# Optimization experiments

Hardware: AMD Instinct MI355X
Metric: run time of the kernel (lower is better)

The kernel has to match this reference:

```python
import jax, jax.numpy as jnp
import numpy as np

UPDATE_SCALE = 1.0
DIST_THRESHOLD = 3.0
W_INJECT = 1.0
W_PIXEL = 1.0
EPS = 1e-8
BIG = 1e6  # sentinel coordinate for masked-out gt points


def extract_zc(sdf):
    """Zero crossings along vertical then horizontal neighbor pairs.
    Returns pts [Ncand,2] float, mask [Ncand] bool (fixed-size, masked)."""
    H, W = sdf.shape
    ii = jnp.arange(H, dtype=sdf.dtype)
    jj = jnp.arange(W, dtype=sdf.dtype)
    # vertical pairs (i,j)-(i+1,j): shape [H-1, W]
    v1, v2 = sdf[:-1, :], sdf[1:, :]
    a = jnp.abs(v1) / (jnp.abs(v1) + jnp.abs(v2) + EPS)
    i0 = ii[:-1, None]
    rv = jnp.where(v1 == 0, i0, jnp.where(v2 == 0, i0 + 1.0, i0 + a))
    cv = jnp.broadcast_to(jj[None, :], v1.shape)
    mv = (v1 == 0) | (v2 == 0) | (v1 * v2 < 0)
    # horizontal pairs (i,j)-(i,j+1): shape [H, W-1]
    h1, h2 = sdf[:, :-1], sdf[:, 1:]
    b = jnp.abs(h1) / (jnp.abs(h1) + jnp.abs(h2) + EPS)
    j0 = jj[None, :-1]
    ch = jnp.where(h1 == 0, j0, jnp.where(h2 == 0, j0 + 1.0, j0 + b))
    rh = jnp.broadcast_to(ii[:, None], h1.shape)
    mh = (h1 == 0) | (h2 == 0) | (h1 * h2 < 0)
    pts = jnp.concatenate([
        jnp.stack([rv.ravel(), cv.ravel()], axis=1),
        jnp.stack([rh.ravel(), ch.ravel()], axis=1)], axis=0)
    mask = jnp.concatenate([mv.ravel(), mh.ravel()], axis=0)
    return pts, mask


def compute_normals(sdf):
    # central differences, one-sided at edges -> [H,W,2]
    gr = jnp.concatenate([sdf[1:2] - sdf[0:1], (sdf[2:] - sdf[:-2]) / 2.0,
                          sdf[-1:] - sdf[-2:-1]], axis=0)
    gc = jnp.concatenate([sdf[:, 1:2] - sdf[:, 0:1], (sdf[:, 2:] - sdf[:, :-2]) / 2.0,
                          sdf[:, -1:] - sdf[:, -2:-1]], axis=1)
    return jnp.stack([gr, gc], axis=2)


def _corners(pts, H, W):
    r, c = pts[:, 0], pts[:, 1]
    r0 = jnp.clip(jnp.floor(r).astype(jnp.int32), 0, H - 1)
    c0 = jnp.clip(jnp.floor(c).astype(jnp.int32), 0, W - 1)
    r1 = jnp.clip(r0 + 1, 0, H - 1)
    c1 = jnp.clip(c0 + 1, 0, W - 1)
    ar = r - r0.astype(r.dtype)
    ac = c - c0.astype(c.dtype)
    wa = (1 - ar) * (1 - ac); wb = (1 - ar) * ac
    wc = ar * (1 - ac); wd = ar * ac
    return r0, c0, r1, c1, wa, wb, wc, wd


def bilinear_gather(img, pts):
    H, W = img.shape[0], img.shape[1]
    r0, c0, r1, c1, wa, wb, wc, wd = _corners(pts, H, W)
    if img.ndim == 3:
        wa, wb, wc, wd = wa[:, None], wb[:, None], wc[:, None], wd[:, None]
    return (img[r0, c0] * wa + img[r0, c1] * wb
            + img[r1, c0] * wc + img[r1, c1] * wd)


def one_image(pred, gt):
    H, W = pred.shape
    gt_pts, gt_m = extract_zc(jax.lax.stop_gradient(gt))
    pr_pts, pr_m = extract_zc(jax.lax.stop_gradient(pred))
    # bilinearly sampled, normalized normals at pred zero crossings
    normals = compute_normals(pred)                         # [H,W,2]
    n = bilinear_gather(normals, pr_pts)                    # [M,2]
    n = n / (jnp.linalg.norm(n, axis=1, keepdims=True) + 1e-8)
    # brute-force NN of each pred ZC point in gt ZC points (masked gt -> far away)
    gp = jnp.where(gt_m[:, None], gt_pts, BIG)              # [N,2]
    d2 = ((pr_pts ** 2).sum(1)[:, None] + (gp ** 2).sum(1)[None, :]
          - 2.0 * pr_pts @ gp.T)                            # [M,N]
    d2 = jnp.maximum(d2, 0.0)
    idx = jnp.argmin(d2, axis=1)
    md2 = jnp.min(d2, axis=1)
    near = gp[idx]                                          # [M,2]
    contrib = pr_m & (md2 <= DIST_THRESHOLD ** 2)
    dirv = near - pr_pts
    dot = jnp.where(contrib, (dirv * n).sum(1) * UPDATE_SCALE, 0.0)
    # bilinear scatter of dot into dSDF (weights vanish exactly where torch skips out-of-range)
    r0, c0, r1, c1, wa, wb, wc, wd = _corners(pr_pts, H, W)
    dSDF = jnp.zeros_like(pred)
    dSDF = (dSDF.at[r0, c0].add(dot * wa)
                 .at[r0, c1].add(dot * wb)
                 .at[r1, c0].add(dot * wc)
                 .at[r1, c1].add(dot * wd))
    dSDF = jax.lax.stop_gradient(dSDF)
    inj = jnp.sum(pred * dSDF)
    vals = bilinear_gather(pred, pr_pts)                    # [M]
    pix = jnp.sum(jnp.where(pr_m, vals, 0.0))
    return inj, pix


def setup_inputs() -> dict:
    key = jax.random.key(0)
    k1, k2 = jax.random.split(key)
    B, H, W = 1, 96, 96
    pred_sdf = jax.random.normal(k1, (B, H, W), dtype=jnp.float32)
    gt_sdf = jax.random.normal(k2, (B, H, W), dtype=jnp.float32)
    return {"pred_sdf": pred_sdf, "gt_sdf": gt_sdf}


def reference(pred_sdf, gt_sdf):
    inj, pix = jax.vmap(one_image)(pred_sdf, gt_sdf)
    inject = inj.mean()
    pixel = pix.mean()
    return W_INJECT * inject + W_PIXEL * pixel
```

## Files before the change

kernel.cpp:

```cpp
#include <hip/hip_runtime.h>
#include <math.h>

#pragma clang fp contract(off)

#define HH 96
#define WW 96
#define NV 9120
#define NC 18240
#define NPIX 9216
#define NCELL 9216
#define SLOTS 6
#define NBLK 4560
#define BIGF 1000000.0f

__global__ void k_prep(const float* __restrict__ PR, const float* __restrict__ GT,
                       float* __restrict__ N,
                       float* prR, float* prC, int* prM,
                       float* gtR, float* gtC,
                       int* counts, float4* cells){
#pragma clang fp contract(off)
  int t = blockIdx.x*256 + threadIdx.x;
  if (t < NPIX){
    int i = t / WW, j = t % WW;
    float gr, gc;
    if (i == 0)         gr = PR[WW+j] - PR[j];
    else if (i == HH-1) gr = PR[(HH-1)*WW+j] - PR[(HH-2)*WW+j];
    else                gr = (PR[(i+1)*WW+j] - PR[(i-1)*WW+j]) / 2.0f;
    if (j == 0)         gc = PR[i*WW+1] - PR[i*WW];
    else if (j == WW-1) gc = PR[i*WW+WW-1] - PR[i*WW+WW-2];
    else                gc = (PR[i*WW+j+1] - PR[i*WW+j-1]) / 2.0f;
    N[t*2] = gr; N[t*2+1] = gc;
  }
  if (t >= 2*NC) return;
  const float* S = (t < NC) ? PR : GT;
  int u = (t < NC) ? t : t - NC;
  float v1, v2, r, c;
  if (u < NV){
    int i0 = u / WW, j = u % WW;
    v1 = S[i0*WW+j]; v2 = S[(i0+1)*WW+j];
    float a1 = fabsf(v1), a2 = fabsf(v2);
    float den = (a1 + a2) + 1e-8f;
    float a = a1 / den;
    float i0f = (float)i0;
    r = (v1 == 0.0f) ? i0f : ((v2 == 0.0f) ? (i0f + 1.0f) : (i0f + a));
    c = (float)j;
  } else {
    int u2 = u - NV;
    int i = u2 / (WW-1), j0 = u2 % (WW-1);
    v1 = S[i*WW+j0]; v2 = S[i*WW+j0+1];
    float a1 = fabsf(v1), a2 = fabsf(v2);
    float den = (a1 + a2) + 1e-8f;
    float b = a1 / den;
    float j0f = (float)j0;
    c = (v1 == 0.0f) ? j0f : ((v2 == 0.0f) ? (j0f + 1.0f) : (j0f + b));
    r = (float)i;
  }
  int m = (v1 == 0.0f) || (v2 == 0.0f) || ((v1*v2) < 0.0f);
  if (t < NC){ prR[u] = r; prC[u] = c; prM[u] = m; }
  else {
    float gr = m ? r : BIGF;
    float gc = m ? c : BIGF;
    gtR[u] = gr; gtC[u] = gc;
    if (m){
      int fr = (int)floorf(r); if (fr < 0) fr = 0; if (fr > HH-1) fr = HH-1;
      int fc = (int)floorf(c); if (fc < 0) fc = 0; if (fc > WW-1) fc = WW-1;
      int cell = fr*WW + fc;
      int slot = atomicAdd(&counts[cell], 1);
      if (slot < SLOTS){
        float sg = (r*r) + (c*c);
        cells[cell*SLOTS + slot] = make_float4(r, c, sg, __int_as_float(u));
      }
    }
  }
}

__global__ __launch_bounds__(256) void k_nndot(
    const float* __restrict__ PR, const float* __restrict__ N,
    const float* __restrict__ prR, const float* __restrict__ prC,
    const int* __restrict__ prM,
    const float* __restrict__ gtR, const float* __restrict__ gtC,
    const int* __restrict__ counts, const float4* __restrict__ cells,
    float* dotA, double* pvPart){
#pragma clang fp contract(off)
  int lane = threadIdx.x & 63, wid = threadIdx.x >> 6;
  int k = blockIdx.x*4 + wid;
  float rp = prR[k], cp = prC[k];
  float sp = (rp*rp) + (cp*cp);
  int fr = (int)floorf(rp), fc = (int)floorf(cp);
  float best = 3.4e38f; int bjg = 0x7fffffff;
  for (int idx = lane; idx < 81; idx += 64){
    int ci = fr + idx/9 - 4;
    int cj = fc + idx%9 - 4;
    if (ci >= 0 && ci < HH && cj >= 0 && cj < WW){
      int cell = ci*WW + cj;
      int n = counts[cell]; if (n > SLOTS) n = SLOTS;
      for (int s = 0; s < n; ++s){
        float4 g = cells[cell*SLOTS + s];
        float cross = fmaf(cp, g.y, rp*g.x);
        float d2 = (sp + g.z) - (2.0f*cross);
        d2 = fmaxf(d2, 0.0f);
        int jg = __float_as_int(g.w);
        if ((d2 < best) || ((d2 == best) && (jg < bjg))){ best = d2; bjg = jg; }
      }
    }
  }
  for (int off = 32; off; off >>= 1){
    float ob = __shfl_xor(best, off, 64);
    int   oj = __shfl_xor(bjg,  off, 64);
    if ((ob < best) || ((ob == best) && (oj < bjg))){ best = ob; bjg = oj; }
  }
  __shared__ double sb[4];
  if (lane == 0){
    if (bjg < 0 || bjg > NC-1) bjg = 0;
    int r0 = (int)floorf(rp); if (r0 < 0) r0 = 0; if (r0 > HH-1) r0 = HH-1;
    int c0 = (int)floorf(cp); if (c0 < 0) c0 = 0; if (c0 > WW-1) c0 = WW-1;
    int r1 = r0 + 1; if (r1 > HH-1) r1 = HH-1;
    int c1 = c0 + 1; if (c1 > WW-1) c1 = WW-1;
    float ar = rp - (float)r0, ac = cp - (float)c0;
    float omr = 1.0f - ar, omc = 1.0f - ac;
    float wa = omr*omc, wb = omr*ac, wc = ar*omc, wd = ar*ac;
    float nr = (((N[(r0*WW+c0)*2]*wa) + (N[(r0*WW+c1)*2]*wb))
               + (N[(r1*WW+c0)*2]*wc)) + (N[(r1*WW+c1)*2]*wd);
    float nc = (((N[(r0*WW+c0)*2+1]*wa) + (N[(r0*WW+c1)*2+1]*wb))
               + (N[(r1*WW+c0)*2+1]*wc)) + (N[(r1*WW+c1)*2+1]*wd);
    float nrm = sqrtf((nr*nr) + (nc*nc));
    float den = nrm + 1e-8f;
    float nru = nr / den, ncu = nc / den;
    float dr = gtR[bjg] - rp;
    float dc = gtC[bjg] - cp;
    float dotv = (dr*nru) + (dc*ncu);
    int m = prM[k];
    int contrib = m && (best <= 9.0f);
    dotA[k] = contrib ? dotv : 0.0f;
    float vals = (((PR[r0*WW+c0]*wa) + (PR[r0*WW+c1]*wb))
                 + (PR[r1*WW+c0]*wc)) + (PR[r1*WW+c1]*wd);
    sb[wid] = m ? (double)vals : 0.0;
  }
  __syncthreads();
  if (threadIdx.x == 0) pvPart[blockIdx.x] = (sb[0]+sb[1])+(sb[2]+sb[3]);
}

__global__ __launch_bounds__(64) void k_pixel(const float* __restrict__ PR,
                        const float* __restrict__ prR, const float* __restrict__ prC,
                        const float* __restrict__ dotA, float* tmp){
#pragma clang fp contract(off)
  int p = blockIdx.x*64 + threadIdx.x;
  if (p >= NPIX) return;
  int i = p / WW, j = p % WW;
  float s = 0.0f;
  for (int i0 = i-1; i0 <= i; ++i0){
    if (i0 < 0 || i0 > HH-2) continue;
    int k = i0*WW + j;
    float r = prR[k];
    int r0 = (int)floorf(r);
    if (r0 == i){
      float ar = r - (float)r0;
      float w = 1.0f - ar;
      s = s + (dotA[k] * w);
    }
  }
  for (int j0 = j-1; j0 <= j; ++j0){
    if (j0 < 0 || j0 > WW-2) continue;
    int k = NV + i*(WW-1) + j0;
    float c = prC[k];
    int c0 = (int)floorf(c);
    if (c0 == j){
      float ac = c - (float)c0;
      float w = 1.0f - ac;
      s = s + (dotA[k] * w);
    }
  }
  for (int j0 = j-2; j0 <= j-1; ++j0){
    if (j0 < 0 || j0 > WW-2) continue;
    int k = NV + i*(WW-1) + j0;
    float c = prC[k];
    int c0 = (int)floorf(c);
    if (c0 == j-1){
      float ac = c - (float)c0;
      s = s + (dotA[k] * ac);
    }
  }
  for (int i0 = i-2; i0 <= i-1; ++i0){
    if (i0 < 0 || i0 > HH-2) continue;
    int k = i0*WW + j;
    float r = prR[k];
    int r0 = (int)floorf(r);
    if (r0 == i-1){
      float ar = r - (float)r0;
      s = s + (dotA[k] * ar);
    }
  }
  tmp[p] = PR[p] * s;
}

__global__ void k_final(const float* __restrict__ tmp,
                        const double* __restrict__ pvPart, float* out){
#pragma clang fp contract(off)
  __shared__ float buf[128];
  __shared__ double dbuf[128];
  int t = threadIdx.x;
  const float4* a4 = (const float4*)(tmp + t*72);
  float4 x = a4[0], y = a4[1];
  float r0=x.x, r1=x.y, r2=x.z, r3=x.w, r4=y.x, r5=y.y, r6=y.z, r7=y.w;
  for (int i4 = 2; i4 < 18; i4 += 2){
    float4 u = a4[i4], v = a4[i4+1];
    r0 += u.x; r1 += u.y; r2 += u.z; r3 += u.w;
    r4 += v.x; r5 += v.y; r6 += v.z; r7 += v.w;
  }
  buf[t] = ((r0+r1)+(r2+r3)) + ((r4+r5)+(r6+r7));
  double pv = 0.0;
  for (int i = t; i < NBLK; i += 128) pv += pvPart[i];
  dbuf[t] = pv;
  __syncthreads();
  for (int st = 1; st < 128; st <<= 1){
    if ((t & (2*st - 1)) == 0){
      buf[t]  = buf[t]  + buf[t+st];
      dbuf[t] = dbuf[t] + dbuf[t+st];
    }
    __syncthreads();
  }
  if (t == 0){
    float inj = buf[0];
    float pix = (float)dbuf[0];
    out[0] = inj + pix;
  }
}

extern "C" void kernel_launch(void* const* d_in, const int* in_sizes, int n_in,
                              void* d_out, int out_size, void* d_ws, size_t ws_size,
                              hipStream_t stream){
  const float* pred = (const float*)d_in[0];
  const float* gt   = (const float*)d_in[1];
  float* out = (float*)d_out;

  float4* cells  = (float4*)((char*)d_ws + 16);
  double* pvPart = (double*)((char*)d_ws + 16 + (size_t)NCELL*SLOTS*sizeof(float4));
  float*  f      = (float*)(pvPart + NBLK);
  float* normals = f;  f += NPIX*2;
  float* prR = f;      f += NC;
  float* prC = f;      f += NC;
  float* gtR = f;      f += NC;
  float* gtC = f;      f += NC;
  float* dotA = f;     f += NC;
  float* tmp = f;      f += NPIX;
  int* prM = (int*)f;  f += NC;
  int* counts = (int*)f;

  hipMemsetAsync(counts, 0, NCELL*sizeof(int), stream);
  k_prep<<<dim3((2*NC+255)/256), dim3(256), 0, stream>>>(pred, gt, normals,
                prR, prC, prM, gtR, gtC, counts, cells);
  k_nndot<<<dim3(NBLK), dim3(256), 0, stream>>>(pred, normals,
                prR, prC, prM, gtR, gtC, counts, cells, dotA, pvPart);
  k_pixel<<<dim3((NPIX+63)/64), dim3(64), 0, stream>>>(pred, prR, prC, dotA, tmp);
  k_final<<<dim3(1), dim3(128), 0, stream>>>(tmp, pvPart, out);
}
```

Before: 88.31 us.

## Build gt cell grid gather-style, shrink NN search window, fuse pixel and final kernels

The gt zero-crossing grid is now built per pixel by gathering its four candidate edges, which removes the memset and the atomics and caps slots at 4. The nearest-neighbour search first scans a 5x5 cell window and only expands to rings 3 and 4 when the best squared distance exceeds about 4. The winning gt coordinates travel with the reduction instead of being re-read from separate arrays. Bilinear normal and value loads are issued up front as float2, and the pixel scatter-gather kernel now does the final reduction via a last-block atomic counter, saving a launch.

```diff
diff --git a/kernel.cpp b/kernel.cpp
--- a/kernel.cpp
+++ b/kernel.cpp
@@ -9,17 +9,18 @@
 #define NC 18240
 #define NPIX 9216
 #define NCELL 9216
-#define SLOTS 6
+#define SLOTS 4
 #define NBLK 4560
+#define PBLK 72
 #define BIGF 1000000.0f
 
-__global__ void k_prep(const float* __restrict__ PR, const float* __restrict__ GT,
-                       float* __restrict__ N,
-                       float* prR, float* prC, int* prM,
-                       float* gtR, float* gtC,
-                       int* counts, float4* cells){
+__global__ __launch_bounds__(256) void k_prep(
+    const float* __restrict__ PR, const float* __restrict__ GT,
+    float2* __restrict__ N2, float* prR, float* prC, int* prM,
+    int* counts, float4* cells, int* finCnt){
 #pragma clang fp contract(off)
   int t = blockIdx.x*256 + threadIdx.x;
+  if (t == 0) *finCnt = 0;
   if (t < NPIX){
     int i = t / WW, j = t % WW;
     float gr, gc;
@@ -29,68 +30,113 @@
     if (j == 0)         gc = PR[i*WW+1] - PR[i*WW];
     else if (j == WW-1) gc = PR[i*WW+WW-1] - PR[i*WW+WW-2];
     else                gc = (PR[i*WW+j+1] - PR[i*WW+j-1]) / 2.0f;
-    N[t*2] = gr; N[t*2+1] = gc;
-  }
-  if (t >= 2*NC) return;
-  const float* S = (t < NC) ? PR : GT;
-  int u = (t < NC) ? t : t - NC;
-  float v1, v2, r, c;
-  if (u < NV){
-    int i0 = u / WW, j = u % WW;
-    v1 = S[i0*WW+j]; v2 = S[(i0+1)*WW+j];
-    float a1 = fabsf(v1), a2 = fabsf(v2);
-    float den = (a1 + a2) + 1e-8f;
-    float a = a1 / den;
-    float i0f = (float)i0;
-    r = (v1 == 0.0f) ? i0f : ((v2 == 0.0f) ? (i0f + 1.0f) : (i0f + a));
-    c = (float)j;
-  } else {
-    int u2 = u - NV;
-    int i = u2 / (WW-1), j0 = u2 % (WW-1);
-    v1 = S[i*WW+j0]; v2 = S[i*WW+j0+1];
-    float a1 = fabsf(v1), a2 = fabsf(v2);
-    float den = (a1 + a2) + 1e-8f;
-    float b = a1 / den;
-    float j0f = (float)j0;
-    c = (v1 == 0.0f) ? j0f : ((v2 == 0.0f) ? (j0f + 1.0f) : (j0f + b));
-    r = (float)i;
-  }
-  int m = (v1 == 0.0f) || (v2 == 0.0f) || ((v1*v2) < 0.0f);
-  if (t < NC){ prR[u] = r; prC[u] = c; prM[u] = m; }
+    N2[t] = make_float2(gr, gc);
+    int cnt = 0;
+    for (int s = 0; s < 2; ++s){
+      int i0 = i - 1 + s;
+      if (i0 >= 0 && i0 <= HH-2){
+        float v1 = GT[i0*WW+j], v2 = GT[(i0+1)*WW+j];
+        int m = (v1 == 0.0f) || (v2 == 0.0f) || ((v1*v2) < 0.0f);
+        if (m){
+          float a1 = fabsf(v1), a2 = fabsf(v2);
+          float den = (a1 + a2) + 1e-8f;
+          float a = a1 / den;
+          float i0f = (float)i0;
+          float r = (v1 == 0.0f) ? i0f : ((v2 == 0.0f) ? (i0f + 1.0f) : (i0f + a));
+          if ((int)floorf(r) == i){
+            float c = (float)j;
+            float sg = (r*r) + (c*c);
+            cells[t*SLOTS + cnt] = make_float4(r, c, sg, __int_as_float(i0*WW+j));
+            cnt++;
+          }
+        }
+      }
+    }
+    for (int s = 0; s < 2; ++s){
+      int j0 = j - 1 + s;
+      if (j0 >= 0 && j0 <= WW-2){
+        float v1 = GT[i*WW+j0], v2 = GT[i*WW+j0+1];
+        int m = (v1 == 0.0f) || (v2 == 0.0f) || ((v1*v2) < 0.0f);
+        if (m){
+          float a1 = fabsf(v1), a2 = fabsf(v2);
+          float den = (a1 + a2) + 1e-8f;
+          float b = a1 / den;
+          float j0f = (float)j0;
+          float c = (v1 == 0.0f) ? j0f : ((v2 == 0.0f) ? (j0f + 1.0f) : (j0f + b));
+          if ((int)floorf(c) == j){
+            float r = (float)i;
+            float sg = (r*r) + (c*c);
+            cells[t*SLOTS + cnt] = make_float4(r, c, sg,
+                                     __int_as_float(NV + i*(WW-1) + j0));
+            cnt++;
+          }
+        }
+      }
+    }
+    counts[t] = cnt;
+  }
+  if (t < NC){
+    float v1, v2, r, c;
+    if (t < NV){
+      int i0 = t / WW, j = t % WW;
+      v1 = PR[i0*WW+j]; v2 = PR[(i0+1)*WW+j];
+      float a1 = fabsf(v1), a2 = fabsf(v2);
+      float den = (a1 + a2) + 1e-8f;
+      float a = a1 / den;
+      float i0f = (float)i0;
+      r = (v1 == 0.0f) ? i0f : ((v2 == 0.0f) ? (i0f + 1.0f) : (i0f + a));
+      c = (float)j;
+    } else {
+      int u2 = t - NV;
+      int i = u2 / (WW-1), j0 = u2 % (WW-1);
+      v1 = PR[i*WW+j0]; v2 = PR[i*WW+j0+1];
+      float a1 = fabsf(v1), a2 = fabsf(v2);
+      float den = (a1 + a2) + 1e-8f;
+      float b = a1 / den;
+      float j0f = (float)j0;
+      c = (v1 == 0.0f) ? j0f : ((v2 == 0.0f) ? (j0f + 1.0f) : (j0f + b));
+      r = (float)i;
+    }
+    prR[t] = r; prC[t] = c;
+    prM[t] = (v1 == 0.0f) || (v2 == 0.0f) || ((v1*v2) < 0.0f);
+  }
+}
+
+__device__ inline void ring_off(int R, int q, int& dr, int& dc){
+  int side = 2*R + 1;
+  if (q < side){ dr = -R; dc = q - R; }
+  else if (q < 2*side){ dr = R; dc = q - side - R; }
   else {
-    float gr = m ? r : BIGF;
-    float gc = m ? c : BIGF;
-    gtR[u] = gr; gtC[u] = gc;
-    if (m){
-      int fr = (int)floorf(r); if (fr < 0) fr = 0; if (fr > HH-1) fr = HH-1;
-      int fc = (int)floorf(c); if (fc < 0) fc = 0; if (fc > WW-1) fc = WW-1;
-      int cell = fr*WW + fc;
-      int slot = atomicAdd(&counts[cell], 1);
-      if (slot < SLOTS){
-        float sg = (r*r) + (c*c);
-        cells[cell*SLOTS + slot] = make_float4(r, c, sg, __int_as_float(u));
-      }
-    }
+    int q2 = q - 2*side, half = side - 2;
+    if (q2 < half){ dr = q2 - R + 1; dc = -R; }
+    else          { dr = q2 - half - R + 1; dc = R; }
   }
 }
 
 __global__ __launch_bounds__(256) void k_nndot(
-    const float* __restrict__ PR, const float* __restrict__ N,
+    const float* __restrict__ PR, const float2* __restrict__ N2,
     const float* __restrict__ prR, const float* __restrict__ prC,
     const int* __restrict__ prM,
-    const float* __restrict__ gtR, const float* __restrict__ gtC,
     const int* __restrict__ counts, const float4* __restrict__ cells,
     float* dotA, double* pvPart){
 #pragma clang fp contract(off)
   int lane = threadIdx.x & 63, wid = threadIdx.x >> 6;
   int k = blockIdx.x*4 + wid;
   float rp = prR[k], cp = prC[k];
+  int m = prM[k];
+  int r0 = (int)floorf(rp); if (r0 < 0) r0 = 0; if (r0 > HH-1) r0 = HH-1;
+  int c0 = (int)floorf(cp); if (c0 < 0) c0 = 0; if (c0 > WW-1) c0 = WW-1;
+  int r1 = r0 + 1; if (r1 > HH-1) r1 = HH-1;
+  int c1 = c0 + 1; if (c1 > WW-1) c1 = WW-1;
+  float2 na = N2[r0*WW+c0], nb = N2[r0*WW+c1];
+  float2 ncn = N2[r1*WW+c0], nd = N2[r1*WW+c1];
+  float pa = PR[r0*WW+c0], pb = PR[r0*WW+c1];
+  float pc = PR[r1*WW+c0], pd = PR[r1*WW+c1];
   float sp = (rp*rp) + (cp*cp);
   int fr = (int)floorf(rp), fc = (int)floorf(cp);
-  float best = 3.4e38f; int bjg = 0x7fffffff;
-  for (int idx = lane; idx < 81; idx += 64){
-    int ci = fr + idx/9 - 4;
-    int cj = fc + idx%9 - 4;
+  float best = 3.4e38f, brg = 0.0f, bcg = 0.0f; int bjg = 0x7fffffff;
+  if (lane < 25){
+    int ci = fr + lane/5 - 2, cj = fc + lane%5 - 2;
     if (ci >= 0 && ci < HH && cj >= 0 && cj < WW){
       int cell = ci*WW + cj;
       int n = counts[cell]; if (n > SLOTS) n = SLOTS;
@@ -100,52 +146,80 @@
         float d2 = (sp + g.z) - (2.0f*cross);
         d2 = fmaxf(d2, 0.0f);
         int jg = __float_as_int(g.w);
-        if ((d2 < best) || ((d2 == best) && (jg < bjg))){ best = d2; bjg = jg; }
+        if ((d2 < best) || ((d2 == best) && (jg < bjg))){
+          best = d2; bjg = jg; brg = g.x; bcg = g.y;
+        }
       }
     }
   }
   for (int off = 32; off; off >>= 1){
     float ob = __shfl_xor(best, off, 64);
     int   oj = __shfl_xor(bjg,  off, 64);
-    if ((ob < best) || ((ob == best) && (oj < bjg))){ best = ob; bjg = oj; }
-  }
+    float orr = __shfl_xor(brg, off, 64);
+    float oc = __shfl_xor(bcg, off, 64);
+    if ((ob < best) || ((ob == best) && (oj < bjg))){
+      best = ob; bjg = oj; brg = orr; bcg = oc;
+    }
+  }
+  if (best > 3.9999f){
+    if (lane < 56){
+      int dr2, dc2;
+      if (lane < 24) ring_off(3, lane, dr2, dc2);
+      else           ring_off(4, lane-24, dr2, dc2);
+      int ci = fr + dr2, cj = fc + dc2;
+      if (ci >= 0 && ci < HH && cj >= 0 && cj < WW){
+        int cell = ci*WW + cj;
+        int n = counts[cell]; if (n > SLOTS) n = SLOTS;
+        for (int s = 0; s < n; ++s){
+          float4 g = cells[cell*SLOTS + s];
+          float cross = fmaf(cp, g.y, rp*g.x);
+          float d2 = (sp + g.z) - (2.0f*cross);
+          d2 = fmaxf(d2, 0.0f);
+          int jg = __float_as_int(g.w);
+          if ((d2 < best) || ((d2 == best) && (jg < bjg))){
+            best = d2; bjg = jg; brg = g.x; bcg = g.y;
+          }
+        }
+      }
+    }
+    for (int off = 32; off; off >>= 1){
+      float ob = __shfl_xor(best, off, 64);
+      int   oj = __shfl_xor(bjg,  off, 64);
+      float orr = __shfl_xor(brg, off, 64);
+      float oc = __shfl_xor(bcg, off, 64);
+      if ((ob < best) || ((ob == best) && (oj < bjg))){
+        best = ob; bjg = oj; brg = orr; bcg = oc;
+      }
+    }
+  }
+  float ar = rp - (float)r0, ac = cp - (float)c0;
+  float omr = 1.0f - ar, omc = 1.0f - ac;
+  float wa = omr*omc, wb = omr*ac, wc = ar*omc, wd = ar*ac;
+  float nr = (((na.x*wa) + (nb.x*wb)) + (ncn.x*wc)) + (nd.x*wd);
+  float nc = (((na.y*wa) + (nb.y*wb)) + (ncn.y*wc)) + (nd.y*wd);
+  float nrm = sqrtf((nr*nr) + (nc*nc));
+  float den = nrm + 1e-8f;
+  float nru = nr / den, ncu = nc / den;
+  float dr = brg - rp, dc = bcg - cp;
+  float dotv = (dr*nru) + (dc*ncu);
+  int contrib = m && (best <= 9.0f);
+  float vals = (((pa*wa) + (pb*wb)) + (pc*wc)) + (pd*wd);
   __shared__ double sb[4];
   if (lane == 0){
-    if (bjg < 0 || bjg > NC-1) bjg = 0;
-    int r0 = (int)floorf(rp); if (r0 < 0) r0 = 0; if (r0 > HH-1) r0 = HH-1;
-    int c0 = (int)floorf(cp); if (c0 < 0) c0 = 0; if (c0 > WW-1) c0 = WW-1;
-    int r1 = r0 + 1; if (r1 > HH-1) r1 = HH-1;
-    int c1 = c0 + 1; if (c1 > WW-1) c1 = WW-1;
-    float ar = rp - (float)r0, ac = cp - (float)c0;
-    float omr = 1.0f - ar, omc = 1.0f - ac;
-    float wa = omr*omc, wb = omr*ac, wc = ar*omc, wd = ar*ac;
-    float nr = (((N[(r0*WW+c0)*2]*wa) + (N[(r0*WW+c1)*2]*wb))
-               + (N[(r1*WW+c0)*2]*wc)) + (N[(r1*WW+c1)*2]*wd);
-    float nc = (((N[(r0*WW+c0)*2+1]*wa) + (N[(r0*WW+c1)*2+1]*wb))
-               + (N[(r1*WW+c0)*2+1]*wc)) + (N[(r1*WW+c1)*2+1]*wd);
-    float nrm = sqrtf((nr*nr) + (nc*nc));
-    float den = nrm + 1e-8f;
-    float nru = nr / den, ncu = nc / den;
-    float dr = gtR[bjg] - rp;
-    float dc = gtC[bjg] - cp;
-    float dotv = (dr*nru) + (dc*ncu);
-    int m = prM[k];
-    int contrib = m && (best <= 9.0f);
     dotA[k] = contrib ? dotv : 0.0f;
-    float vals = (((PR[r0*WW+c0]*wa) + (PR[r0*WW+c1]*wb))
-                 + (PR[r1*WW+c0]*wc)) + (PR[r1*WW+c1]*wd);
     sb[wid] = m ? (double)vals : 0.0;
   }
   __syncthreads();
   if (threadIdx.x == 0) pvPart[blockIdx.x] = (sb[0]+sb[1])+(sb[2]+sb[3]);
 }
 
-__global__ __launch_bounds__(64) void k_pixel(const float* __restrict__ PR,
-                        const float* __restrict__ prR, const float* __restrict__ prC,
-                        const float* __restrict__ dotA, float* tmp){
+__global__ __launch_bounds__(128) void k_pixfinal(
+    const float* __restrict__ PR,
+    const float* __restrict__ prR, const float* __restrict__ prC,
+    const float* __restrict__ dotA, const double* __restrict__ pvPart,
+    float* tmp, int* finCnt, float* out){
 #pragma clang fp contract(off)
-  int p = blockIdx.x*64 + threadIdx.x;
-  if (p >= NPIX) return;
+  int p = blockIdx.x*128 + threadIdx.x;
   int i = p / WW, j = p % WW;
   float s = 0.0f;
   for (int i0 = i-1; i0 <= i; ++i0){
@@ -191,25 +265,30 @@
     }
   }
   tmp[p] = PR[p] * s;
-}
-
-__global__ void k_final(const float* __restrict__ tmp,
-                        const double* __restrict__ pvPart, float* out){
-#pragma clang fp contract(off)
+  __threadfence();
+  __syncthreads();
+  __shared__ int lastFlag;
+  if (threadIdx.x == 0){
+    int old = atomicAdd(finCnt, 1);
+    lastFlag = (old == PBLK-1);
+  }
+  __syncthreads();
+  if (!lastFlag) return;
+  __threadfence();
   __shared__ float buf[128];
   __shared__ double dbuf[128];
   int t = threadIdx.x;
   const float4* a4 = (const float4*)(tmp + t*72);
   float4 x = a4[0], y = a4[1];
-  float r0=x.x, r1=x.y, r2=x.z, r3=x.w, r4=y.x, r5=y.y, r6=y.z, r7=y.w;
+  float q0=x.x, q1=x.y, q2=x.z, q3=x.w, q4=y.x, q5=y.y, q6=y.z, q7=y.w;
   for (int i4 = 2; i4 < 18; i4 += 2){
     float4 u = a4[i4], v = a4[i4+1];
-    r0 += u.x; r1 += u.y; r2 += u.z; r3 += u.w;
-    r4 += v.x; r5 += v.y; r6 += v.z; r7 += v.w;
-  }
-  buf[t] = ((r0+r1)+(r2+r3)) + ((r4+r5)+(r6+r7));
+    q0 += u.x; q1 += u.y; q2 += u.z; q3 += u.w;
+    q4 += v.x; q5 += v.y; q6 += v.z; q7 += v.w;
+  }
+  buf[t] = ((q0+q1)+(q2+q3)) + ((q4+q5)+(q6+q7));
   double pv = 0.0;
-  for (int i = t; i < NBLK; i += 128) pv += pvPart[i];
+  for (int idx = t; idx < NBLK; idx += 128) pv += pvPart[idx];
   dbuf[t] = pv;
   __syncthreads();
   for (int st = 1; st < 128; st <<= 1){
@@ -219,11 +298,7 @@
     }
     __syncthreads();
   }
-  if (t == 0){
-    float inj = buf[0];
-    float pix = (float)dbuf[0];
-    out[0] = inj + pix;
-  }
+  if (t == 0) out[0] = buf[0] + (float)dbuf[0];
 }
 
 extern "C" void kernel_launch(void* const* d_in, const int* in_sizes, int n_in,
@@ -233,24 +308,22 @@
   const float* gt   = (const float*)d_in[1];
   float* out = (float*)d_out;
 
-  float4* cells  = (float4*)((char*)d_ws + 16);
-  double* pvPart = (double*)((char*)d_ws + 16 + (size_t)NCELL*SLOTS*sizeof(float4));
-  float*  f      = (float*)(pvPart + NBLK);
-  float* normals = f;  f += NPIX*2;
-  float* prR = f;      f += NC;
-  float* prC = f;      f += NC;
-  float* gtR = f;      f += NC;
-  float* gtC = f;      f += NC;
-  float* dotA = f;     f += NC;
-  float* tmp = f;      f += NPIX;
-  int* prM = (int*)f;  f += NC;
-  int* counts = (int*)f;
-
-  hipMemsetAsync(counts, 0, NCELL*sizeof(int), stream);
-  k_prep<<<dim3((2*NC+255)/256), dim3(256), 0, stream>>>(pred, gt, normals,
-                prR, prC, prM, gtR, gtC, counts, cells);
-  k_nndot<<<dim3(NBLK), dim3(256), 0, stream>>>(pred, normals,
-                prR, prC, prM, gtR, gtC, counts, cells, dotA, pvPart);
-  k_pixel<<<dim3((NPIX+63)/64), dim3(64), 0, stream>>>(pred, prR, prC, dotA, tmp);
-  k_final<<<dim3(1), dim3(128), 0, stream>>>(tmp, pvPart, out);
-}
+  char* w = (char*)d_ws;
+  float4* cells  = (float4*)w;                 w += (size_t)NCELL*SLOTS*sizeof(float4);
+  double* pvPart = (double*)w;                 w += (size_t)NBLK*sizeof(double);
+  float2* N2     = (float2*)w;                 w += (size_t)NPIX*sizeof(float2);
+  float*  prR    = (float*)w;                  w += (size_t)NC*sizeof(float);
+  float*  prC    = (float*)w;                  w += (size_t)NC*sizeof(float);
+  float*  dotA   = (float*)w;                  w += (size_t)NC*sizeof(float);
+  float*  tmp    = (float*)w;                  w += (size_t)NPIX*sizeof(float);
+  int*    prM    = (int*)w;                    w += (size_t)NC*sizeof(int);
+  int*    counts = (int*)w;                    w += (size_t)NCELL*sizeof(int);
+  int*    finCnt = (int*)w;
+
+  k_prep<<<dim3(72), dim3(256), 0, stream>>>(pred, gt, N2, prR, prC, prM,
+                                             counts, cells, finCnt);
+  k_nndot<<<dim3(NBLK), dim3(256), 0, stream>>>(pred, N2, prR, prC, prM,
+                                                counts, cells, dotA, pvPart);
+  k_pixfinal<<<dim3(PBLK), dim3(128), 0, stream>>>(pred, prR, prC, dotA,
+                                                   pvPart, tmp, finCnt, out);
+}
```

After: 84.65 us. 1.04x faster.
